# Performance work log

Hardware: AMD Instinct MI355X
Metric: run time of the kernel (lower is better)

## Reference

```python
import jax, jax.numpy as jnp
import numpy as np

N_HEAD = 12


def setup_inputs() -> dict:
    key = jax.random.key(0)
    ks = jax.random.split(key, 6)
    B, T, C = 8, 1024, 768
    x = jax.random.normal(ks[0], (B, T, C), dtype=jnp.float32)
    w_attn = jax.random.normal(ks[1], (C, 3 * C), dtype=jnp.float32) * 0.02
    b_attn = jnp.zeros((3 * C,), dtype=jnp.float32)
    w_proj = jax.random.normal(ks[2], (C, C), dtype=jnp.float32) * 0.02
    b_proj = jnp.zeros((C,), dtype=jnp.float32)
    rel_emb = jax.random.normal(ks[3], (2 * 1024 - 1, C // N_HEAD), dtype=jnp.float32) * 0.02
    return {"x": x, "w_attn": w_attn, "b_attn": b_attn,
            "w_proj": w_proj, "b_proj": b_proj, "rel_emb": rel_emb}


def reference(x, w_attn, b_attn, w_proj, b_proj, rel_emb):
    b, t, c = x.shape
    h = N_HEAD
    d = c // h
    scale = d ** -0.5
    # fused QKV projection
    qkv = x @ w_attn + b_attn                       # [b, t, 3c]
    q, k, v = jnp.split(qkv, 3, axis=-1)
    split_heads = lambda z: z.reshape(b, t, h, d).transpose(0, 2, 1, 3)  # [b,h,t,d]
    q, k, v = map(split_heads, (q, k, v))
    q = q * scale
    # content scores
    scores = jnp.einsum('bhid,bhjd->bhij', q, k)    # [b,h,t,t]
    # relative position bias: embed lookup + rel-shift (zero row prepended, last dropped)
    rel = rel_emb[:t]                               # [t, d]
    rel = jnp.concatenate([jnp.zeros_like(rel[:1]), rel], axis=0)[:-1]
    scores = scores + jnp.einsum('bhid,jd->bhij', q, rel)
    # causal mask
    causal = jnp.tril(jnp.ones((t, t), dtype=bool))
    scores = jnp.where(causal, scores, -jnp.inf)
    probs = jax.nn.softmax(scores, axis=-1)
    y = jnp.einsum('bhij,bhjd->bhid', probs, v)     # [b,h,t,d]
    y = y.transpose(0, 2, 1, 3).reshape(b, t, c)
    return y @ w_proj + b_proj
```

## Files before the change

kernel.cpp:

```cpp
#include <hip/hip_runtime.h>
#include <stdint.h>


typedef __attribute__((ext_vector_type(8))) short short8;
typedef __attribute__((ext_vector_type(4))) float f32x4;
typedef __attribute__((ext_vector_type(4))) unsigned short ushort4v;

#define DEV static __device__ __forceinline__

DEV float bf2f(unsigned short u) {
    union { unsigned int u; float f; } v; v.u = ((unsigned int)u) << 16; return v.f;
}
DEV unsigned short f2bf(float f) {
    union { float f; unsigned int u; } v; v.f = f;
    unsigned int u = v.u;
    return (unsigned short)((u + 0x7fffu + ((u >> 16) & 1u)) >> 16);
}

typedef const __attribute__((address_space(1))) void* gas_ptr;
typedef __attribute__((address_space(3))) void* las_ptr;
DEV void glds16(const void* g, void* l) {
    __builtin_amdgcn_global_load_lds((gas_ptr)g, (las_ptr)l, 16, 0, 0);
}

__global__ void detect_dtype(const unsigned int* __restrict__ w, int* __restrict__ flag) {
    __shared__ int cnt;
    if (threadIdx.x == 0) cnt = 0;
    __syncthreads();
    int c = 0;
    for (int i = threadIdx.x; i < 8192; i += 256) {
        unsigned int b1 = (w[i] >> 8) & 0x7F;
        c += (b1 >= 0x38 && b1 <= 0x3E) ? 1 : 0;
    }
    atomicAdd(&cnt, c);
    __syncthreads();
    if (threadIdx.x == 0) *flag = (cnt > 4096) ? 1 : 0;
}

__global__ __launch_bounds__(256) void cast_x(
    const void* __restrict__ x, unsigned short* __restrict__ xo,
    const int* __restrict__ flag)
{
    int i = (blockIdx.x * 256 + threadIdx.x) * 4;
    if (*flag) {
        *(ushort4v*)(xo + i) = *(const ushort4v*)((const unsigned short*)x + i);
    } else {
        f32x4 v = *(const f32x4*)((const float*)x + i);
        ushort4v o;
#pragma unroll
        for (int j = 0; j < 4; ++j) o[j] = f2bf(v[j]);
        *(ushort4v*)(xo + i) = o;
    }
}

__global__ __launch_bounds__(256) void cast_small(
    const void* __restrict__ rel, const void* __restrict__ ba, const void* __restrict__ bp,
    unsigned short* __restrict__ rel_o, unsigned short* __restrict__ ba_o,
    unsigned short* __restrict__ bp_o, const int* __restrict__ flag)
{
    int i = blockIdx.x * 256 + threadIdx.x;
    if (i >= 134080) return;
    int isbf = *flag;
    const void* src; unsigned short* dst; int off;
    if (i < 131008)      { src = rel; dst = rel_o; off = i; }
    else if (i < 133312) { src = ba;  dst = ba_o;  off = i - 131008; }
    else                 { src = bp;  dst = bp_o;  off = i - 133312; }
    dst[off] = isbf ? ((const unsigned short*)src)[off]
                    : f2bf(((const float*)src)[off]);
}

__global__ __launch_bounds__(256) void transpose_w(
    const void* __restrict__ in, unsigned short* __restrict__ out,
    int R, int C, const int* __restrict__ flag)
{
    __shared__ unsigned short tile[64][66];
    const int t = threadIdx.x;
    const int cb = blockIdx.x * 64;
    const int rb = blockIdx.y * 64;
    if (*flag) {
        const unsigned short* inp = (const unsigned short*)in;
        const int c8 = (t & 7) * 8;
        const int r = t >> 3;
#pragma unroll
        for (int p = 0; p < 2; ++p) {
            int rr = r + p * 32;
            short8 v = *(const short8*)(inp + (size_t)(rb + rr) * C + cb + c8);
#pragma unroll
            for (int i = 0; i < 8; ++i) tile[rr][c8 + i] = (unsigned short)v[i];
        }
    } else {
        const float* inp = (const float*)in;
        const int c4 = (t & 15) * 4;
        const int r = t >> 4;
#pragma unroll
        for (int p = 0; p < 4; ++p) {
            int rr = r + p * 16;
            f32x4 v = *(const f32x4*)(inp + (size_t)(rb + rr) * C + cb + c4);
#pragma unroll
            for (int i = 0; i < 4; ++i) tile[rr][c4 + i] = f2bf(v[i]);
        }
    }
    __syncthreads();
    {
        const int c8 = (t & 7) * 8;
        const int r = t >> 3;
#pragma unroll
        for (int p = 0; p < 2; ++p) {
            int oc = r + p * 32;
            short8 v;
#pragma unroll
            for (int i = 0; i < 8; ++i) v[i] = (short)tile[c8 + i][oc];
            *(short8*)(out + (size_t)(cb + oc) * R + rb + c8) = v;
        }
    }
}

#define GEMM_PROLOG(A_, Bt_)                                                     \
    __shared__ __align__(16) unsigned short Abuf[2][128 * 32];                   \
    __shared__ __align__(16) unsigned short Bbuf[2][128 * 32];                   \
    const int t = threadIdx.x;                                                   \
    const int wave = t >> 6, lane = t & 63;                                      \
    const int lo = lane & 15, hi = lane >> 4;                                    \
    const int wr = wave >> 1, wc = wave & 1;                                     \
    const int bm = blockIdx.x * 128;                                             \
    const int bn = blockIdx.y * 128;                                             \
    int L0 = t << 4, L1 = (t + 256) << 4;                                        \
    int S0 = L0 ^ (((L0 >> 7) & 3) << 4);                                        \
    int S1 = L1 ^ (((L1 >> 7) & 3) << 4);                                        \
    int r0 = S0 >> 6, o0 = (S0 & 63) >> 1;                                       \
    int r1 = S1 >> 6, o1 = (S1 & 63) >> 1;                                       \
    const unsigned short* Ab = (A_) + (size_t)bm * 768;                          \
    const unsigned short* Bb = (Bt_) + (size_t)bn * 768;                         \
    const int lof0 = (wave * 64) << 4;                                           \
    const int lof1 = (256 + wave * 64) << 4;                                     \
    int aoff[4]; int boff[4];                                                    \
    _Pragma("unroll")                                                            \
    for (int m = 0; m < 4; ++m) {                                                \
        int Pa = ((wr * 64 + m * 16 + lo) << 6) + (hi << 4);                     \
        aoff[m] = Pa ^ (((Pa >> 7) & 3) << 4);                                   \
        int Pb = ((wc * 64 + m * 16 + lo) << 6) + (hi << 4);                     \
        boff[m] = Pb ^ (((Pb >> 7) & 3) << 4);                                   \
    }                                                                            \
    f32x4 acc[4][4];                                                             \
    _Pragma("unroll")                                                            \
    for (int m = 0; m < 4; ++m)                                                  \
        _Pragma("unroll")                                                        \
        for (int n = 0; n < 4; ++n) acc[m][n] = (f32x4){0.f, 0.f, 0.f, 0.f};     \
                                         \
    glds16(Ab + (size_t)r0 * 768 + o0, (char*)Abuf[0] + lof0);                   \
    glds16(Ab + (size_t)r1 * 768 + o1, (char*)Abuf[0] + lof1);                   \
    glds16(Bb + (size_t)r0 * 768 + o0, (char*)Bbuf[0] + lof0);                   \
    glds16(Bb + (size_t)r1 * 768 + o1, (char*)Bbuf[0] + lof1);                   \
    int cur = 0;                                                                 \
    for (int k0 = 0; k0 < 768; k0 += 32) {                                       \
        __syncthreads();        \
        if (k0 + 32 < 768) {                                                     \
            const int kn = k0 + 32;                                              \
            glds16(Ab + (size_t)r0 * 768 + kn + o0, (char*)Abuf[cur ^ 1] + lof0);\
            glds16(Ab + (size_t)r1 * 768 + kn + o1, (char*)Abuf[cur ^ 1] + lof1);\
            glds16(Bb + (size_t)r0 * 768 + kn + o0, (char*)Bbuf[cur ^ 1] + lof0);\
            glds16(Bb + (size_t)r1 * 768 + kn + o1, (char*)Bbuf[cur ^ 1] + lof1);\
        }                                                                        \
        short8 af[4], bfv[4];                                                    \
        _Pragma("unroll")                                                        \
        for (int m = 0; m < 4; ++m)                                              \
            af[m] = *(const short8*)((const char*)Abuf[cur] + aoff[m]);          \
        _Pragma("unroll")                                                        \
        for (int n = 0; n < 4; ++n)                                              \
            bfv[n] = *(const short8*)((const char*)Bbuf[cur] + boff[n]);         \
        _Pragma("unroll")                                                        \
        for (int m = 0; m < 4; ++m)                                              \
            _Pragma("unroll")                                                    \
            for (int n = 0; n < 4; ++n)                                          \
                acc[m][n] = __builtin_amdgcn_mfma_f32_16x16x32_bf16(             \
                    af[m], bfv[n], acc[m][n], 0, 0, 0);                          \
        cur ^= 1;                                                                \
    }

__global__ __launch_bounds__(256) void gemm_qkv(
    const unsigned short* __restrict__ A,
    const unsigned short* __restrict__ Bt,
    const unsigned short* __restrict__ bias,
    const unsigned short* __restrict__ rel,
    unsigned short* __restrict__ q_ws,
    unsigned short* __restrict__ k_ws,
    unsigned short* __restrict__ v_ws)
{
    GEMM_PROLOG(A, Bt)
    const int gm0 = bm + wr * 64 + hi * 4;
    const float QSCALE = 0.125f * 1.44269504f;
#pragma unroll
    for (int m = 0; m < 4; ++m) {
        int gm = gm0 + m * 16;
        int b_ = gm >> 10;
        int tt = gm & 1023;
#pragma unroll
        for (int n = 0; n < 4; ++n) {
            int col = bn + wc * 64 + n * 16 + lo;
            float bs = bf2f(bias[col]);
            if (col < 768) {
                int h = col >> 6, d = col & 63;
                size_t base = (((size_t)b_ * 12 + h) * 1024 + tt) * 64 + d;
#pragma unroll
                for (int j = 0; j < 4; ++j)
                    q_ws[base + (size_t)j * 64] = f2bf((acc[m][n][j] + bs) * QSCALE);
            } else if (col < 1536) {
                int h = (col - 768) >> 6, d = col & 63;
                size_t base = (((size_t)b_ * 12 + h) * 1024 + tt) * 64 + d;
#pragma unroll
                for (int j = 0; j < 4; ++j) {
                    int trow = tt + j;
                    float rv = (trow > 0) ? bf2f(rel[(size_t)(trow - 1) * 64 + d]) : 0.f;
                    k_ws[base + (size_t)j * 64] = f2bf(acc[m][n][j] + bs + rv);
                }
            } else {
                int h = (col - 1536) >> 6, d = col & 63;
                size_t vb = (((size_t)b_ * 12 + h) * 64 + d) * 1024 + tt;
                ushort4v pk;
#pragma unroll
                for (int j = 0; j < 4; ++j) pk[j] = f2bf(acc[m][n][j] + bs);
                *(ushort4v*)(v_ws + vb) = pk;
            }
        }
    }
}

__global__ __launch_bounds__(256) void gemm_proj(
    const unsigned short* __restrict__ A,
    const unsigned short* __restrict__ Bt,
    const unsigned short* __restrict__ bias,
    const int* __restrict__ flag,
    void* __restrict__ outv)
{
    GEMM_PROLOG(A, Bt)
    const int isbf = *flag;
    const int gm0 = bm + wr * 64 + hi * 4;
#pragma unroll
    for (int m = 0; m < 4; ++m) {
        int gm = gm0 + m * 16;
#pragma unroll
        for (int n = 0; n < 4; ++n) {
            int col = bn + wc * 64 + n * 16 + lo;
            float bs = bf2f(bias[col]);
#pragma unroll
            for (int j = 0; j < 4; ++j) {
                float v = acc[m][n][j] + bs;
                if (isbf)
                    ((unsigned short*)outv)[(size_t)(gm + j) * 768 + col] = f2bf(v);
                else
                    ((float*)outv)[(size_t)(gm + j) * 768 + col] = v;
            }
        }
    }
}

__global__ __launch_bounds__(256) void attn_fused(
    const unsigned short* __restrict__ q_ws,
    const unsigned short* __restrict__ k_ws,
    const unsigned short* __restrict__ v_ws,
    unsigned short* __restrict__ att)
{
    __shared__ __align__(16) unsigned short Kbuf[2][64 * 64];
    __shared__ __align__(16) unsigned short Vbuf[2][64 * 64];
    __shared__ __align__(16) unsigned short Pbuf[4][16 * 64];
    const int t = threadIdx.x;
    const int wave = t >> 6, lane = t & 63;
    const int lo = lane & 15, hi = lane >> 4;
    const int gid = blockIdx.x;
    const int xcd = gid & 7;
    const int c = gid >> 3;
    const int bh = xcd * 12 + (c % 12);
    const int pairIdx = c / 12;
    const int b_ = bh / 12, h = bh % 12;
    const size_t base = (size_t)bh * (1024 * 64);
    const unsigned short* Kb = k_ws + base;
    const unsigned short* Vb = v_ws + base;
    const float DEFER_THR = 11.5f;

    int L0 = t << 4, L1 = (t + 256) << 4;
    int S0 = L0 ^ (((L0 >> 7) & 7) << 4);
    int S1 = L1 ^ (((L1 >> 7) & 7) << 4);
    int r0 = S0 >> 7, o0 = (S0 & 127) >> 1;
    int r1 = S1 >> 7, o1 = (S1 & 127) >> 1;
    const int lof0 = (wave * 64) << 4;
    const int lof1 = (256 + wave * 64) << 4;

    int koff[4][2];
#pragma unroll
    for (int nt = 0; nt < 4; ++nt)
#pragma unroll
        for (int kc = 0; kc < 2; ++kc) {
            int P = ((nt * 16 + lo) << 7) + (kc << 6) + (hi << 4);
            koff[nt][kc] = P ^ (((P >> 7) & 7) << 4);
        }
    int poffR[2];
#pragma unroll
    for (int kc = 0; kc < 2; ++kc) {
        int P = (lo << 7) + (kc << 6) + (hi << 4);
        poffR[kc] = P ^ (((P >> 7) & 7) << 4);
    }
    int poffW[4][4];
#pragma unroll
    for (int nt = 0; nt < 4; ++nt)
#pragma unroll
        for (int j = 0; j < 4; ++j) {
            int P = (lo << 7) + ((nt * 16 + hi * 4 + j) << 1);
            poffW[nt][j] = P ^ ((lo & 7) << 4);
        }
    char* pb = (char*)&Pbuf[wave][0];

#pragma unroll 1
    for (int sel = 0; sel < 2; ++sel) {
        const int qt = sel ? pairIdx : (15 - pairIdx);
        const int q0w = qt * 64 + wave * 16;
        const int qrow = q0w + lo;

        short8 qf[2];
#pragma unroll
        for (int kc = 0; kc < 2; ++kc)
            qf[kc] = *(const short8*)(q_ws + base +
                (size_t)(q0w + lo) * 64 + kc * 32 + hi * 8);

        f32x4 o[4];
        float mrun = -1e30f, lrun = 0.f;
#pragma unroll
        for (int nt = 0; nt < 4; ++nt) o[nt] = (f32x4){0.f, 0.f, 0.f, 0.f};

        if (sel) __syncthreads();
        glds16(Kb + (size_t)r0 * 64 + o0, (char*)Kbuf[0] + lof0);
        glds16(Kb + (size_t)r1 * 64 + o1, (char*)Kbuf[0] + lof1);
        glds16(Vb + (size_t)r0 * 1024 + o0, (char*)Vbuf[0] + lof0);
        glds16(Vb + (size_t)r1 * 1024 + o1, (char*)Vbuf[0] + lof1);

        int cur = 0;
        const int nkt = qt + 1;
        for (int kt = 0; kt < nkt; ++kt) {
            __syncthreads();
            if (kt + 1 < nkt) {
                const int kn = (kt + 1) * 64;
                glds16(Kb + (size_t)(kn + r0) * 64 + o0, (char*)Kbuf[cur ^ 1] + lof0);
                glds16(Kb + (size_t)(kn + r1) * 64 + o1, (char*)Kbuf[cur ^ 1] + lof1);
                glds16(Vb + (size_t)r0 * 1024 + kn + o0, (char*)Vbuf[cur ^ 1] + lof0);
                glds16(Vb + (size_t)r1 * 1024 + kn + o1, (char*)Vbuf[cur ^ 1] + lof1);
            }
            const int kv0 = kt * 64;
            const char* Kc = (const char*)Kbuf[cur];
            const char* Vc = (const char*)Vbuf[cur];

            short8 kf[4][2];
#pragma unroll
            for (int nt = 0; nt < 4; ++nt)
#pragma unroll
                for (int kc = 0; kc < 2; ++kc)
                    kf[nt][kc] = *(const short8*)(Kc + koff[nt][kc]);
            f32x4 sc[4];
            __builtin_amdgcn_s_setprio(1);
#pragma unroll
            for (int nt = 0; nt < 4; ++nt) {
                f32x4 z = (f32x4){0.f, 0.f, 0.f, 0.f};
                z = __builtin_amdgcn_mfma_f32_16x16x32_bf16(kf[nt][0], qf[0], z, 0, 0, 0);
                z = __builtin_amdgcn_mfma_f32_16x16x32_bf16(kf[nt][1], qf[1], z, 0, 0, 0);
                sc[nt] = z;
            }
            __builtin_amdgcn_s_setprio(0);
            if (kv0 + 63 > q0w) {
#pragma unroll
                for (int nt = 0; nt < 4; ++nt)
#pragma unroll
                    for (int j = 0; j < 4; ++j) {
                        int kc_ = kv0 + nt * 16 + hi * 4 + j;
                        if (kc_ > qrow) sc[nt][j] = -1e30f;
                    }
            }
            float m0;
            {
                float a0 = fmaxf(fmaxf(sc[0][0], sc[0][1]), fmaxf(sc[0][2], sc[0][3]));
                float a1 = fmaxf(fmaxf(sc[1][0], sc[1][1]), fmaxf(sc[1][2], sc[1][3]));
                float a2 = fmaxf(fmaxf(sc[2][0], sc[2][1]), fmaxf(sc[2][2], sc[2][3]));
                float a3 = fmaxf(fmaxf(sc[3][0], sc[3][1]), fmaxf(sc[3][2], sc[3][3]));
                m0 = fmaxf(fmaxf(a0, a1), fmaxf(a2, a3));
            }
            m0 = fmaxf(m0, __shfl_xor(m0, 16));
            m0 = fmaxf(m0, __shfl_xor(m0, 32));
            if (__any(m0 > mrun + DEFER_THR)) {
                float nm = fmaxf(mrun, m0);
                float corr = __builtin_amdgcn_exp2f(mrun - nm);
                mrun = nm;
                lrun *= corr;
#pragma unroll
                for (int j = 0; j < 4; ++j) {
                    float cj = __shfl(corr, hi * 4 + j);
#pragma unroll
                    for (int nt = 0; nt < 4; ++nt) o[nt][j] *= cj;
                }
            }
            float rs = 0.f;
#pragma unroll
            for (int nt = 0; nt < 4; ++nt)
#pragma unroll
                for (int j = 0; j < 4; ++j) {
                    float p = __builtin_amdgcn_exp2f(sc[nt][j] - mrun);
                    sc[nt][j] = p;
                    rs += p;
                }
            rs += __shfl_xor(rs, 16);
            rs += __shfl_xor(rs, 32);
            lrun += rs;
            short8 vf[4][2];
#pragma unroll
            for (int nt = 0; nt < 4; ++nt)
#pragma unroll
                for (int kc2 = 0; kc2 < 2; ++kc2)
                    vf[nt][kc2] = *(const short8*)(Vc + koff[nt][kc2]);
#pragma unroll
            for (int nt = 0; nt < 4; ++nt)
#pragma unroll
                for (int j = 0; j < 4; ++j)
                    *(unsigned short*)(pb + poffW[nt][j]) = f2bf(sc[nt][j]);
#pragma unroll
            for (int kc2 = 0; kc2 < 2; ++kc2) {
                short8 pf = *(const short8*)(pb + poffR[kc2]);
                __builtin_amdgcn_s_setprio(1);
#pragma unroll
                for (int nt = 0; nt < 4; ++nt)
                    o[nt] = __builtin_amdgcn_mfma_f32_16x16x32_bf16(pf, vf[nt][kc2], o[nt], 0, 0, 0);
                __builtin_amdgcn_s_setprio(0);
            }
            cur ^= 1;
        }
#pragma unroll
        for (int j = 0; j < 4; ++j) {
            float lj = __shfl(lrun, hi * 4 + j);
            float inv = 1.f / lj;
            int tt = q0w + hi * 4 + j;
#pragma unroll
            for (int nt = 0; nt < 4; ++nt)
                att[((size_t)(b_ * 1024 + tt)) * 768 + h * 64 + nt * 16 + lo] =
                    f2bf(o[nt][j] * inv);
        }
    }
}

extern "C" void kernel_launch(void* const* d_in, const int* in_sizes, int n_in,
                              void* d_out, int out_size, void* d_ws, size_t ws_size,
                              hipStream_t stream) {
    const void* x      = d_in[0];
    const void* w_attn = d_in[1];
    const void* b_attn = d_in[2];
    const void* w_proj = d_in[3];
    const void* b_proj = d_in[4];
    const void* rel    = d_in[5];
    char* ws = (char*)d_ws;
    int*            flag = (int*)(ws + 0);
    unsigned short* wTa  = (unsigned short*)(ws + 4096);
    unsigned short* wTp  = (unsigned short*)(ws + 3543040);
    unsigned short* x_bf = (unsigned short*)(ws + 4722688);
    unsigned short* relb = (unsigned short*)(ws + 17305600);
    unsigned short* bab  = (unsigned short*)(ws + 17567616);
    unsigned short* bpb  = (unsigned short*)(ws + 17572224);
    unsigned short* q_ws = (unsigned short*)(ws + 17573760);
    unsigned short* k_ws = (unsigned short*)(ws + 30156672);
    unsigned short* v_ws = (unsigned short*)(ws + 42739584);
    unsigned short* att  = x_bf;

    detect_dtype<<<1, 256, 0, stream>>>((const unsigned int*)w_attn, flag);
    cast_x<<<6144, 256, 0, stream>>>(x, x_bf, flag);
    cast_small<<<524, 256, 0, stream>>>(rel, b_attn, b_proj, relb, bab, bpb, flag);
    transpose_w<<<dim3(36, 12), 256, 0, stream>>>(w_attn, wTa, 768, 2304, flag);
    transpose_w<<<dim3(12, 12), 256, 0, stream>>>(w_proj, wTp, 768, 768, flag);
    gemm_qkv<<<dim3(64, 18), 256, 0, stream>>>(x_bf, wTa, bab, relb, q_ws, k_ws, v_ws);
    attn_fused<<<768, 256, 0, stream>>>(q_ws, k_ws, v_ws, att);
    gemm_proj<<<dim3(64, 6), 256, 0, stream>>>(att, wTp, bpb, flag, (void*)d_out);
}
```

Measured before the change: 214.2 us.

## Triple-buffer GEMM K-loop with explicit vmcnt waits and raw barriers

New measurement: 206.1 us. 1.04x faster.

```diff
diff --git a/kernel.cpp b/kernel.cpp
--- a/kernel.cpp
+++ b/kernel.cpp
@@ -115,9 +115,15 @@
     }
 }
 
+#define GEMM_STAGE(kk, sl)                                                       \
+    glds16(Ab + (size_t)r0 * 768 + (kk) + o0, (char*)Abuf[sl] + lof0);           \
+    glds16(Ab + (size_t)r1 * 768 + (kk) + o1, (char*)Abuf[sl] + lof1);           \
+    glds16(Bb + (size_t)r0 * 768 + (kk) + o0, (char*)Bbuf[sl] + lof0);           \
+    glds16(Bb + (size_t)r1 * 768 + (kk) + o1, (char*)Bbuf[sl] + lof1);
+
 #define GEMM_PROLOG(A_, Bt_)                                                     \
-    __shared__ __align__(16) unsigned short Abuf[2][128 * 32];                   \
-    __shared__ __align__(16) unsigned short Bbuf[2][128 * 32];                   \
+    __shared__ __align__(16) unsigned short Abuf[3][128 * 32];                   \
+    __shared__ __align__(16) unsigned short Bbuf[3][128 * 32];                   \
     const int t = threadIdx.x;                                                   \
     const int wave = t >> 6, lane = t & 63;                                      \
     const int lo = lane & 15, hi = lane >> 4;                                    \
@@ -146,35 +152,28 @@
     for (int m = 0; m < 4; ++m)                                                  \
         _Pragma("unroll")                                                        \
         for (int n = 0; n < 4; ++n) acc[m][n] = (f32x4){0.f, 0.f, 0.f, 0.f};     \
-                                         \
-    glds16(Ab + (size_t)r0 * 768 + o0, (char*)Abuf[0] + lof0);                   \
-    glds16(Ab + (size_t)r1 * 768 + o1, (char*)Abuf[0] + lof1);                   \
-    glds16(Bb + (size_t)r0 * 768 + o0, (char*)Bbuf[0] + lof0);                   \
-    glds16(Bb + (size_t)r1 * 768 + o1, (char*)Bbuf[0] + lof1);                   \
-    int cur = 0;                                                                 \
-    for (int k0 = 0; k0 < 768; k0 += 32) {                                       \
-        __syncthreads();        \
-        if (k0 + 32 < 768) {                                                     \
-            const int kn = k0 + 32;                                              \
-            glds16(Ab + (size_t)r0 * 768 + kn + o0, (char*)Abuf[cur ^ 1] + lof0);\
-            glds16(Ab + (size_t)r1 * 768 + kn + o1, (char*)Abuf[cur ^ 1] + lof1);\
-            glds16(Bb + (size_t)r0 * 768 + kn + o0, (char*)Bbuf[cur ^ 1] + lof0);\
-            glds16(Bb + (size_t)r1 * 768 + kn + o1, (char*)Bbuf[cur ^ 1] + lof1);\
-        }                                                                        \
+    GEMM_STAGE(0, 0)                                                             \
+    GEMM_STAGE(32, 1)                                                            \
+    _Pragma("unroll")                                                            \
+    for (int kt_ = 0; kt_ < 24; ++kt_) {                                         \
+        if (kt_ < 23) { asm volatile("s_waitcnt vmcnt(4)" ::: "memory"); }       \
+        else          { asm volatile("s_waitcnt vmcnt(0)" ::: "memory"); }       \
+        __builtin_amdgcn_s_barrier();                                            \
+        if (kt_ + 2 < 24) { GEMM_STAGE((kt_ + 2) * 32, (kt_ + 2) % 3) }          \
+        const int cur_ = kt_ % 3;                                                \
         short8 af[4], bfv[4];                                                    \
         _Pragma("unroll")                                                        \
         for (int m = 0; m < 4; ++m)                                              \
-            af[m] = *(const short8*)((const char*)Abuf[cur] + aoff[m]);          \
+            af[m] = *(const short8*)((const char*)Abuf[cur_] + aoff[m]);         \
         _Pragma("unroll")                                                        \
         for (int n = 0; n < 4; ++n)                                              \
-            bfv[n] = *(const short8*)((const char*)Bbuf[cur] + boff[n]);         \
+            bfv[n] = *(const short8*)((const char*)Bbuf[cur_] + boff[n]);        \
         _Pragma("unroll")                                                        \
         for (int m = 0; m < 4; ++m)                                              \
             _Pragma("unroll")                                                    \
             for (int n = 0; n < 4; ++n)                                          \
                 acc[m][n] = __builtin_amdgcn_mfma_f32_16x16x32_bf16(             \
                     af[m], bfv[n], acc[m][n], 0, 0, 0);                          \
-        cur ^= 1;                                                                \
     }
 
 __global__ __launch_bounds__(256) void gemm_qkv(
```
